# Kernel optimization log

Measured on AMD Instinct MI355X. Metric: run time of the kernel, lower is better.

## Reference

```python
import jax, jax.numpy as jnp
import numpy as np

H, W, C = 192, 192, 1024

def setup_inputs() -> dict:
    key = jax.random.key(0)
    k1, k2 = jax.random.split(key)
    x = jax.random.normal(k1, (1, H, W, C), dtype=jnp.float32)
    gamma = jax.random.normal(k2, (1,), dtype=jnp.float32)
    return {"x": x, "gamma": gamma}

def reference(x, gamma):
    b, h, w, c = x.shape
    # NOTE: faithful to the TF code: a pure reshape of NHWC into (1, C, H*W),
    # with NO transpose (the original relies on reshape semantics).
    proj = x.reshape(1, c, h * w)                      # query == key^T == value
    energy = jnp.einsum('bcn,bdn->bcd', proj, proj)    # (1, C, C)
    energy_new = jnp.max(energy, axis=-1, keepdims=True) - energy  # sign-flipped
    attention = jax.nn.softmax(energy_new, axis=-1)    # (1, C, C)
    out = jnp.einsum('bcd,bdn->bcn', attention, proj)  # (1, C, H*W)
    out = out.reshape(1, h, w, c)
    return gamma * out + x
```

## Files before the change

### kernel.cpp

```cpp
#include <hip/hip_runtime.h>
#include <cstdint>

#define C_DIM 1024
#define N_DIM 36864

typedef unsigned short ushort_t;
typedef __attribute__((ext_vector_type(8))) short bf16x8;
typedef __attribute__((ext_vector_type(4))) float f32x4;

__device__ __forceinline__ ushort_t f2b(float f) {
    unsigned u = __float_as_uint(f);
    u = (u + 0x7fffu + ((u >> 16) & 1u)) >> 16;
    return (ushort_t)u;
}
__device__ __forceinline__ float b2f(ushort_t b) {
    return __uint_as_float(((unsigned)b) << 16);
}

__device__ __forceinline__ void async16(const void* g, const void* lds) {
    __builtin_amdgcn_global_load_lds(
        (const __attribute__((address_space(1))) unsigned int*)(uintptr_t)g,
        (__attribute__((address_space(3))) unsigned int*)(uint32_t)(uintptr_t)lds,
        16, 0, 0);
}

__global__ __launch_bounds__(256) void k_convert(const float* __restrict__ x,
                                                 ushort_t* __restrict__ ph,
                                                 ushort_t* __restrict__ pl) {
    int i = blockIdx.x * 256 + threadIdx.x;
    float4 v = ((const float4*)x)[i];
    ushort4 h, l;
    h.x = f2b(v.x); l.x = f2b(v.x - b2f(h.x));
    h.y = f2b(v.y); l.y = f2b(v.y - b2f(h.y));
    h.z = f2b(v.z); l.z = f2b(v.z - b2f(h.z));
    h.w = f2b(v.w); l.w = f2b(v.w - b2f(h.w));
    ((ushort4*)ph)[i] = h;
    ((ushort4*)pl)[i] = l;
}

__global__ __launch_bounds__(256) void k_egemm(const ushort_t* __restrict__ ph,
                                               const ushort_t* __restrict__ pl,
                                               float* __restrict__ g1,
                                               float* __restrict__ g2,
                                               int kchunk) {
    __shared__ __align__(16) ushort_t sA [128 * 32];
    __shared__ __align__(16) ushort_t sBh[64 * 32];
    __shared__ __align__(16) ushort_t sBl[64 * 32];

    const int t = threadIdx.x;
    const int w = t >> 6;
    const int L = t & 63;
    const int c0 = blockIdx.x << 7;
    const int d0 = blockIdx.y << 6;
    const int kb = blockIdx.z * kchunk;

    const int lrow = L >> 2, lcol = (L & 3) << 3;

    const ushort_t* gA0 = ph + (size_t)(c0 + (w << 5) + lrow) * N_DIM + kb + lcol;
    const ushort_t* gB0 = (w < 2 ? ph : pl) +
                          (size_t)(d0 + ((w & 1) << 5) + lrow) * N_DIM + kb + lcol;
    ushort_t* lA0 = sA + ((w << 5) << 5);
    ushort_t* lB0 = (w < 2 ? sBh : sBl) + (((w & 1) << 5) << 5);

    const int wm = (w >> 1) << 6;
    const int wn = (w & 1) << 5;
    const int lm = L & 15, q = L >> 4;

    f32x4 acc1[4][2], acc2[4][2];
#pragma unroll
    for (int a = 0; a < 4; ++a)
#pragma unroll
        for (int b = 0; b < 2; ++b) { acc1[a][b] = (f32x4)0.0f; acc2[a][b] = (f32x4)0.0f; }

    for (int kk = 0; kk < kchunk; kk += 32) {
        async16(gA0,                 lA0);
        async16(gA0 + 16 * N_DIM,    lA0 + 16 * 32);
        async16(gB0,                 lB0);
        async16(gB0 + 16 * N_DIM,    lB0 + 16 * 32);
        gA0 += 32; gB0 += 32;
        __syncthreads();

        bf16x8 a[4], bh[2], bl[2];
#pragma unroll
        for (int mt = 0; mt < 4; ++mt)
            a[mt] = *(const bf16x8*)(sA + ((wm + (mt << 4) + lm) << 5) + (q << 3));
#pragma unroll
        for (int nt = 0; nt < 2; ++nt) {
            bh[nt] = *(const bf16x8*)(sBh + ((wn + (nt << 4) + lm) << 5) + (q << 3));
            bl[nt] = *(const bf16x8*)(sBl + ((wn + (nt << 4) + lm) << 5) + (q << 3));
        }
#pragma unroll
        for (int mt = 0; mt < 4; ++mt)
#pragma unroll
            for (int nt = 0; nt < 2; ++nt) {
                acc1[mt][nt] = __builtin_amdgcn_mfma_f32_16x16x32_bf16(a[mt], bh[nt], acc1[mt][nt], 0, 0, 0);
                acc2[mt][nt] = __builtin_amdgcn_mfma_f32_16x16x32_bf16(a[mt], bl[nt], acc2[mt][nt], 0, 0, 0);
            }
        __syncthreads();
    }

    const size_t zb = (size_t)blockIdx.z << 20;
#pragma unroll
    for (int mt = 0; mt < 4; ++mt)
#pragma unroll
        for (int nt = 0; nt < 2; ++nt)
#pragma unroll
            for (int r = 0; r < 4; ++r) {
                int cg = c0 + wm + (mt << 4) + (q << 2) + r;
                int dg = d0 + wn + (nt << 4) + lm;
                size_t o = zb + ((size_t)cg << 10) + dg;
                g1[o] = acc1[mt][nt][r];
                g2[o] = acc2[mt][nt][r];
            }
}

__global__ __launch_bounds__(256) void k_reduce(const float* __restrict__ g1,
                                                const float* __restrict__ g2,
                                                float* __restrict__ E,
                                                int splitk) {
    __shared__ float ld[64][65];
    const int t = threadIdx.x;
    const int i = t >> 2;
    const int jb = (t & 3) << 4;
    const int c0 = blockIdx.y << 6;
    const int d0 = blockIdx.x << 6;

    float acc[16];
#pragma unroll
    for (int u = 0; u < 16; ++u) acc[u] = 0.0f;

    for (int z = 0; z < splitk; ++z) {
        const size_t zb = (size_t)z << 20;
        const float* p1 = g1 + zb + ((size_t)(c0 + i) << 10) + d0 + jb;
        const float* p2 = g2 + zb + ((size_t)(c0 + i) << 10) + d0 + jb;
        const float* pt = g2 + zb + ((size_t)(d0 + i) << 10) + c0 + jb;
#pragma unroll
        for (int u4 = 0; u4 < 4; ++u4) {
            float4 v1 = ((const float4*)p1)[u4];
            float4 v2 = ((const float4*)p2)[u4];
            acc[u4 * 4 + 0] += v1.x + v2.x;
            acc[u4 * 4 + 1] += v1.y + v2.y;
            acc[u4 * 4 + 2] += v1.z + v2.z;
            acc[u4 * 4 + 3] += v1.w + v2.w;
        }
        __syncthreads();
#pragma unroll
        for (int u4 = 0; u4 < 4; ++u4)
            *(float4*)&ld[i][jb + u4 * 4] = ((const float4*)pt)[u4];
        __syncthreads();
#pragma unroll
        for (int u = 0; u < 16; ++u)
            acc[u] += ld[jb + u][i];
    }

    float* eo = E + ((size_t)(c0 + i) << 10) + d0 + jb;
#pragma unroll
    for (int u4 = 0; u4 < 4; ++u4) {
        float4 v;
        v.x = acc[u4 * 4 + 0]; v.y = acc[u4 * 4 + 1];
        v.z = acc[u4 * 4 + 2]; v.w = acc[u4 * 4 + 3];
        ((float4*)eo)[u4] = v;
    }
}

__global__ __launch_bounds__(256) void k_softmax(const float* __restrict__ E,
                                                 ushort_t* __restrict__ att) {
    const int c = blockIdx.x;
    const int t = threadIdx.x;
    __shared__ float red[4];
    __shared__ float bcast;

    float4 e4 = ((const float4*)E)[((size_t)c << 8) + t];
    float m = fminf(fminf(e4.x, e4.y), fminf(e4.z, e4.w));
#pragma unroll
    for (int off = 32; off > 0; off >>= 1) m = fminf(m, __shfl_down(m, off));
    if ((t & 63) == 0) red[t >> 6] = m;
    __syncthreads();
    if (t == 0) bcast = fminf(fminf(red[0], red[1]), fminf(red[2], red[3]));
    __syncthreads();
    m = bcast;

    float w0 = expf(m - e4.x), w1 = expf(m - e4.y);
    float w2 = expf(m - e4.z), w3 = expf(m - e4.w);
    float s = w0 + w1 + w2 + w3;
#pragma unroll
    for (int off = 32; off > 0; off >>= 1) s += __shfl_down(s, off);
    if ((t & 63) == 0) red[t >> 6] = s;
    __syncthreads();
    if (t == 0) bcast = red[0] + red[1] + red[2] + red[3];
    __syncthreads();
    float inv = 1.0f / bcast;
    ushort4 o;
    o.x = f2b(w0 * inv); o.y = f2b(w1 * inv);
    o.z = f2b(w2 * inv); o.w = f2b(w3 * inv);
    ((ushort4*)att)[((size_t)c << 8) + t] = o;
}

__global__ __launch_bounds__(256) void k_transpose(const ushort_t* __restrict__ ph,
                                                   ushort_t* __restrict__ pht) {
    __shared__ __align__(16) ushort_t tile[64][72];
    const int t = threadIdx.x;
    const int i = t >> 2, qd = t & 3;
    const int c0 = blockIdx.y << 6;
    const size_t n0 = (size_t)blockIdx.x << 6;

    const ushort_t* src = ph + (size_t)(c0 + i) * N_DIM + n0 + (qd << 4);
    uint4 v0 = *(const uint4*)src;
    uint4 v1 = *(const uint4*)(src + 8);
    *(uint4*)&tile[i][qd << 4]       = v0;
    *(uint4*)&tile[i][(qd << 4) + 8] = v1;
    __syncthreads();

    ushort_t tmp[16];
#pragma unroll
    for (int u = 0; u < 16; ++u) tmp[u] = tile[(qd << 4) + u][i];
    ushort_t* dst = pht + (n0 + i) * C_DIM + c0 + (qd << 4);
    *(uint4*)dst       = *(uint4*)tmp;
    *(uint4*)(dst + 8) = *(uint4*)(tmp + 8);
}

__global__ __launch_bounds__(256) void k_ogemm(const ushort_t* __restrict__ att,
                                               const ushort_t* __restrict__ pht,
                                               const float* __restrict__ x,
                                               const float* __restrict__ gamma,
                                               float* __restrict__ out) {
    __shared__ __align__(16) ushort_t sA[128 * 32];
    __shared__ __align__(16) ushort_t sB[128 * 32];

    const int t = threadIdx.x;
    const int w = t >> 6, L = t & 63;
    const int n0 = blockIdx.x << 7;
    const int c0 = blockIdx.y << 7;
    const int srow = L >> 2, scol = (L & 3) << 3;

    const int wm = (w >> 1) << 6, wn = (w & 1) << 6;
    const int lm = L & 15, q = L >> 4;

    f32x4 acc[4][4];
#pragma unroll
    for (int a = 0; a < 4; ++a)
#pragma unroll
        for (int b = 0; b < 4; ++b) acc[a][b] = (f32x4)0.0f;

    for (int k = 0; k < C_DIM; k += 32) {
#pragma unroll
        for (int j = 0; j < 4; ++j) {
            int ch = (w << 2) + j;
            int row = ((ch & 7) << 4) + srow;
            const ushort_t* src = (ch < 8)
                ? att + (size_t)(c0 + row) * C_DIM + k + scol
                : pht + (size_t)(n0 + row) * C_DIM + k + scol;
            ushort_t* base = (ch < 8) ? sA : sB;
            async16(src, base + (((ch & 7) << 4) << 5));
        }
        __syncthreads();

        bf16x8 a[4], b[4];
#pragma unroll
        for (int mt = 0; mt < 4; ++mt)
            a[mt] = *(const bf16x8*)(sA + ((wm + (mt << 4) + lm) << 5) + (q << 3));
#pragma unroll
        for (int nt = 0; nt < 4; ++nt)
            b[nt] = *(const bf16x8*)(sB + ((wn + (nt << 4) + lm) << 5) + (q << 3));
#pragma unroll
        for (int mt = 0; mt < 4; ++mt)
#pragma unroll
            for (int nt = 0; nt < 4; ++nt)
                acc[mt][nt] = __builtin_amdgcn_mfma_f32_16x16x32_bf16(a[mt], b[nt], acc[mt][nt], 0, 0, 0);
        __syncthreads();
    }

    const float g = gamma[0];
#pragma unroll
    for (int mt = 0; mt < 4; ++mt)
#pragma unroll
        for (int nt = 0; nt < 4; ++nt)
#pragma unroll
            for (int r = 0; r < 4; ++r) {
                int cg = c0 + wm + (mt << 4) + (q << 2) + r;
                int ng = n0 + wn + (nt << 4) + lm;
                size_t o = (size_t)cg * N_DIM + ng;
                out[o] = g * acc[mt][nt][r] + x[o];
            }
}

extern "C" void kernel_launch(void* const* d_in, const int* in_sizes, int n_in,
                              void* d_out, int out_size, void* d_ws, size_t ws_size,
                              hipStream_t stream) {
    const float* x     = (const float*)d_in[0];
    const float* gamma = (const float*)d_in[1];
    float* out = (float*)d_out;
    char* ws = (char*)d_ws;

    const size_t PH = 75497472ull, SLICE = 4194304ull, EB = 4194304ull, AT = 2097152ull;
    int S = 8;
    if (ws_size < 2 * PH + (size_t)S * 2 * SLICE + EB + AT) S = 4;
    if (ws_size < 2 * PH + (size_t)S * 2 * SLICE + EB + AT) S = 3;
    const int kchunk = N_DIM / S;

    ushort_t* ph  = (ushort_t*)(ws);
    ushort_t* pl  = (ushort_t*)(ws + PH);
    float*    g1  = (float*)   (ws + 2 * PH);
    float*    g2  = (float*)   (ws + 2 * PH + (size_t)S * SLICE);
    float*    E   = (float*)   (ws + 2 * PH + (size_t)S * 2 * SLICE);
    ushort_t* att = (ushort_t*)(ws + 2 * PH + (size_t)S * 2 * SLICE + EB);
    ushort_t* pht = pl;

    k_convert<<<dim3((C_DIM * (size_t)N_DIM / 4) / 256), 256, 0, stream>>>(x, ph, pl);

    k_egemm<<<dim3(8, 16, S), 256, 0, stream>>>(ph, pl, g1, g2, kchunk);

    k_reduce<<<dim3(16, 16), 256, 0, stream>>>(g1, g2, E, S);

    k_softmax<<<dim3(C_DIM), 256, 0, stream>>>(E, att);

    k_transpose<<<dim3(N_DIM / 64, C_DIM / 64), 256, 0, stream>>>(ph, pht);

    k_ogemm<<<dim3(N_DIM / 128, C_DIM / 128), 256, 0, stream>>>(att, pht, x, gamma, out);
}
```

Baseline: 697.3 us.

## Fuse bf16 split conversion with transpose and double-buffer energy GEMM LDS

Adds a k_convtrans kernel that writes the hi/lo bf16 split and the transposed hi copy in a single pass over x. This removes the separate transpose kernel and its re-read of ph, and it is used only when the workspace has room for a third P-sized buffer. The energy GEMM now double-buffers its LDS tiles and issues the next tile's async loads before computing on the current one. It waits with explicit s_waitcnt vmcnt plus raw barriers instead of __syncthreads, which doubles LDS use and depends on the hand-coded waitcnt values being correct.

```diff
diff --git a/kernel.cpp b/kernel.cpp
--- a/kernel.cpp
+++ b/kernel.cpp
@@ -38,14 +38,52 @@
     ((ushort4*)pl)[i] = l;
 }
 
+__global__ __launch_bounds__(256) void k_convtrans(const float* __restrict__ x,
+                                                   ushort_t* __restrict__ ph,
+                                                   ushort_t* __restrict__ pl,
+                                                   ushort_t* __restrict__ pht) {
+    __shared__ __align__(16) ushort_t th[64][72];
+    const int t = threadIdx.x;
+    const int i = t >> 2, qd = t & 3;
+    const int c0 = blockIdx.y << 6;
+    const size_t n0 = (size_t)blockIdx.x << 6;
+
+    const size_t row = (size_t)(c0 + i) * N_DIM + n0 + (qd << 4);
+    const float* src = x + row;
+    union { ushort_t s[16]; uint4 q[2]; } H, Lo;
+#pragma unroll
+    for (int u4 = 0; u4 < 4; ++u4) {
+        float4 v = ((const float4*)src)[u4];
+        ushort_t h0 = f2b(v.x), h1 = f2b(v.y), h2 = f2b(v.z), h3 = f2b(v.w);
+        H.s[u4 * 4 + 0] = h0; Lo.s[u4 * 4 + 0] = f2b(v.x - b2f(h0));
+        H.s[u4 * 4 + 1] = h1; Lo.s[u4 * 4 + 1] = f2b(v.y - b2f(h1));
+        H.s[u4 * 4 + 2] = h2; Lo.s[u4 * 4 + 2] = f2b(v.z - b2f(h2));
+        H.s[u4 * 4 + 3] = h3; Lo.s[u4 * 4 + 3] = f2b(v.w - b2f(h3));
+    }
+    *(uint4*)(ph + row)     = H.q[0];
+    *(uint4*)(ph + row + 8) = H.q[1];
+    *(uint4*)(pl + row)     = Lo.q[0];
+    *(uint4*)(pl + row + 8) = Lo.q[1];
+    *(uint4*)&th[i][qd << 4]       = H.q[0];
+    *(uint4*)&th[i][(qd << 4) + 8] = H.q[1];
+    __syncthreads();
+
+    ushort_t tmp[16];
+#pragma unroll
+    for (int u = 0; u < 16; ++u) tmp[u] = th[(qd << 4) + u][i];
+    ushort_t* dst = pht + (n0 + i) * C_DIM + c0 + (qd << 4);
+    *(uint4*)dst       = *(uint4*)tmp;
+    *(uint4*)(dst + 8) = *(uint4*)(tmp + 8);
+}
+
 __global__ __launch_bounds__(256) void k_egemm(const ushort_t* __restrict__ ph,
                                                const ushort_t* __restrict__ pl,
                                                float* __restrict__ g1,
                                                float* __restrict__ g2,
                                                int kchunk) {
-    __shared__ __align__(16) ushort_t sA [128 * 32];
-    __shared__ __align__(16) ushort_t sBh[64 * 32];
-    __shared__ __align__(16) ushort_t sBl[64 * 32];
+    __shared__ __align__(16) ushort_t sA [2][128 * 32];
+    __shared__ __align__(16) ushort_t sBh[2][64 * 32];
+    __shared__ __align__(16) ushort_t sBl[2][64 * 32];
 
     const int t = threadIdx.x;
     const int w = t >> 6;
@@ -53,14 +91,14 @@
     const int c0 = blockIdx.x << 7;
     const int d0 = blockIdx.y << 6;
     const int kb = blockIdx.z * kchunk;
-
     const int lrow = L >> 2, lcol = (L & 3) << 3;
 
     const ushort_t* gA0 = ph + (size_t)(c0 + (w << 5) + lrow) * N_DIM + kb + lcol;
     const ushort_t* gB0 = (w < 2 ? ph : pl) +
                           (size_t)(d0 + ((w & 1) << 5) + lrow) * N_DIM + kb + lcol;
-    ushort_t* lA0 = sA + ((w << 5) << 5);
-    ushort_t* lB0 = (w < 2 ? sBh : sBl) + (((w & 1) << 5) << 5);
+    ushort_t* lA[2] = { sA[0] + ((w << 5) << 5), sA[1] + ((w << 5) << 5) };
+    ushort_t* lB[2] = { (w < 2 ? sBh[0] : sBl[0]) + (((w & 1) << 5) << 5),
+                        (w < 2 ? sBh[1] : sBl[1]) + (((w & 1) << 5) << 5) };
 
     const int wm = (w >> 1) << 6;
     const int wn = (w & 1) << 5;
@@ -72,22 +110,36 @@
 #pragma unroll
         for (int b = 0; b < 2; ++b) { acc1[a][b] = (f32x4)0.0f; acc2[a][b] = (f32x4)0.0f; }
 
-    for (int kk = 0; kk < kchunk; kk += 32) {
-        async16(gA0,                 lA0);
-        async16(gA0 + 16 * N_DIM,    lA0 + 16 * 32);
-        async16(gB0,                 lB0);
-        async16(gB0 + 16 * N_DIM,    lB0 + 16 * 32);
-        gA0 += 32; gB0 += 32;
-        __syncthreads();
+    auto stage = [&](int ti, int b) {
+        const ushort_t* ga = gA0 + (ti << 5);
+        const ushort_t* gb = gB0 + (ti << 5);
+        async16(ga,              lA[b]);
+        async16(ga + 16 * N_DIM, lA[b] + 16 * 32);
+        async16(gb,              lB[b]);
+        async16(gb + 16 * N_DIM, lB[b] + 16 * 32);
+    };
+
+    const int nIter = kchunk >> 5;
+    stage(0, 0);
+
+    for (int ti = 0; ti < nIter; ++ti) {
+        const int cb = ti & 1;
+        if (ti + 1 < nIter) {
+            stage(ti + 1, cb ^ 1);
+            __builtin_amdgcn_s_waitcnt(0x0F74);
+        } else {
+            __builtin_amdgcn_s_waitcnt(0x0F70);
+        }
+        __builtin_amdgcn_s_barrier();
 
         bf16x8 a[4], bh[2], bl[2];
 #pragma unroll
         for (int mt = 0; mt < 4; ++mt)
-            a[mt] = *(const bf16x8*)(sA + ((wm + (mt << 4) + lm) << 5) + (q << 3));
+            a[mt] = *(const bf16x8*)(sA[cb] + ((wm + (mt << 4) + lm) << 5) + (q << 3));
 #pragma unroll
         for (int nt = 0; nt < 2; ++nt) {
-            bh[nt] = *(const bf16x8*)(sBh + ((wn + (nt << 4) + lm) << 5) + (q << 3));
-            bl[nt] = *(const bf16x8*)(sBl + ((wn + (nt << 4) + lm) << 5) + (q << 3));
+            bh[nt] = *(const bf16x8*)(sBh[cb] + ((wn + (nt << 4) + lm) << 5) + (q << 3));
+            bl[nt] = *(const bf16x8*)(sBl[cb] + ((wn + (nt << 4) + lm) << 5) + (q << 3));
         }
 #pragma unroll
         for (int mt = 0; mt < 4; ++mt)
@@ -96,7 +148,7 @@
                 acc1[mt][nt] = __builtin_amdgcn_mfma_f32_16x16x32_bf16(a[mt], bh[nt], acc1[mt][nt], 0, 0, 0);
                 acc2[mt][nt] = __builtin_amdgcn_mfma_f32_16x16x32_bf16(a[mt], bl[nt], acc2[mt][nt], 0, 0, 0);
             }
-        __syncthreads();
+        __builtin_amdgcn_s_barrier();
     }
 
     const size_t zb = (size_t)blockIdx.z << 20;
@@ -292,29 +344,44 @@
     float* out = (float*)d_out;
     char* ws = (char*)d_ws;
 
-    const size_t PH = 75497472ull, SLICE = 4194304ull, EB = 4194304ull, AT = 2097152ull;
+    const size_t P = 75497472ull, SL = 4194304ull, EB = 4194304ull, AT = 2097152ull;
+
     int S = 8;
-    if (ws_size < 2 * PH + (size_t)S * 2 * SLICE + EB + AT) S = 4;
-    if (ws_size < 2 * PH + (size_t)S * 2 * SLICE + EB + AT) S = 3;
+    bool fused = (ws_size >= 3 * P + (size_t)S * 2 * SL + EB + AT);
+    if (!fused) {
+        if (ws_size < 2 * P + (size_t)S * 2 * SL + EB + AT) S = 4;
+        if (ws_size < 2 * P + (size_t)S * 2 * SL + EB + AT) S = 3;
+    }
     const int kchunk = N_DIM / S;
 
-    ushort_t* ph  = (ushort_t*)(ws);
-    ushort_t* pl  = (ushort_t*)(ws + PH);
-    float*    g1  = (float*)   (ws + 2 * PH);
-    float*    g2  = (float*)   (ws + 2 * PH + (size_t)S * SLICE);
-    float*    E   = (float*)   (ws + 2 * PH + (size_t)S * 2 * SLICE);
-    ushort_t* att = (ushort_t*)(ws + 2 * PH + (size_t)S * 2 * SLICE + EB);
-    ushort_t* pht = pl;
-
-    k_convert<<<dim3((C_DIM * (size_t)N_DIM / 4) / 256), 256, 0, stream>>>(x, ph, pl);
-
-    k_egemm<<<dim3(8, 16, S), 256, 0, stream>>>(ph, pl, g1, g2, kchunk);
-
-    k_reduce<<<dim3(16, 16), 256, 0, stream>>>(g1, g2, E, S);
-
-    k_softmax<<<dim3(C_DIM), 256, 0, stream>>>(E, att);
-
-    k_transpose<<<dim3(N_DIM / 64, C_DIM / 64), 256, 0, stream>>>(ph, pht);
-
-    k_ogemm<<<dim3(N_DIM / 128, C_DIM / 128), 256, 0, stream>>>(att, pht, x, gamma, out);
-}
+    if (fused) {
+        ushort_t* ph  = (ushort_t*)(ws);
+        ushort_t* pl  = (ushort_t*)(ws + P);
+        ushort_t* pht = (ushort_t*)(ws + 2 * P);
+        float*    g1  = (float*)   (ws + 3 * P);
+        float*    g2  = (float*)   (ws + 3 * P + (size_t)S * SL);
+        float*    E   = (float*)   (ws + 3 * P + (size_t)S * 2 * SL);
+        ushort_t* att = (ushort_t*)(ws + 3 * P + (size_t)S * 2 * SL + EB);
+
+        k_convtrans<<<dim3(N_DIM / 64, C_DIM / 64), 256, 0, stream>>>(x, ph, pl, pht);
+        k_egemm<<<dim3(8, 16, S), 256, 0, stream>>>(ph, pl, g1, g2, kchunk);
+        k_reduce<<<dim3(16, 16), 256, 0, stream>>>(g1, g2, E, S);
+        k_softmax<<<dim3(C_DIM), 256, 0, stream>>>(E, att);
+        k_ogemm<<<dim3(N_DIM / 128, C_DIM / 128), 256, 0, stream>>>(att, pht, x, gamma, out);
+    } else {
+        ushort_t* ph  = (ushort_t*)(ws);
+        ushort_t* pl  = (ushort_t*)(ws + P);
+        float*    g1  = (float*)   (ws + 2 * P);
+        float*    g2  = (float*)   (ws + 2 * P + (size_t)S * SL);
+        float*    E   = (float*)   (ws + 2 * P + (size_t)S * 2 * SL);
+        ushort_t* att = (ushort_t*)(ws + 2 * P + (size_t)S * 2 * SL + EB);
+        ushort_t* pht = pl;
+
+        k_convert<<<dim3((C_DIM * (size_t)N_DIM / 4) / 256), 256, 0, stream>>>(x, ph, pl);
+        k_egemm<<<dim3(8, 16, S), 256, 0, stream>>>(ph, pl, g1, g2, kchunk);
+        k_reduce<<<dim3(16, 16), 256, 0, stream>>>(g1, g2, E, S);
+        k_softmax<<<dim3(C_DIM), 256, 0, stream>>>(E, att);
+        k_transpose<<<dim3(N_DIM / 64, C_DIM / 64), 256, 0, stream>>>(ph, pht);
+        k_ogemm<<<dim3(N_DIM / 128, C_DIM / 128), 256, 0, stream>>>(att, pht, x, gamma, out);
+    }
+}
```

Result: faster. 681.0 us (-2.3%).
